# Performance work log

Measured on AMD Instinct MI355X. Metric: run time of the kernel, lower is better.

Reference implementation:

```python
import jax, jax.numpy as jnp
import numpy as np

EPS = 1e-5          # denominator epsilon from module
PROJ_EPS = 4e-3     # geoopt float32 projection epsilon
MIN_NORM = 1e-15


def _sabs(x):
    return jnp.abs(x) + MIN_NORM


def _sign(x):
    # geoopt sign: sign(0) == 1
    return jnp.sign(jnp.sign(x) + 0.5)


def _clamp_abs(x, eps):
    return _sign(x) * jnp.maximum(jnp.abs(x), eps)


def _lambda_x(x, k):
    # conformal factor 2 / (1 + k ||x||^2)
    return 2.0 / jnp.maximum(1.0 + k * jnp.sum(x * x, axis=-1, keepdims=True), MIN_NORM)


def _parallel_transport0back(x, v, k):
    # transport v at x back to the origin: v / (1 + k ||x||^2)
    return v / jnp.maximum(1.0 + k * jnp.sum(x * x, axis=-1, keepdims=True), MIN_NORM)


def _artan_k(x, k):
    sk = jnp.sqrt(_sabs(k))
    hyp = jnp.arctanh(jnp.minimum(sk * x, 1.0 - 1e-7)) / sk   # k < 0
    sph = jnp.arctan(sk * x) / sk                              # k > 0
    return jnp.where(k < 0, hyp, sph)


def _tan_k(x, k):
    sk = jnp.sqrt(_sabs(k))
    return jnp.where(k < 0, jnp.tanh(sk * x) / sk, jnp.tan(sk * x) / sk)


def _project(x, k):
    maxnorm = (1.0 - PROJ_EPS) / jnp.sqrt(_sabs(k))
    maxnorm = jnp.where(k < 0, maxnorm, 1e15)
    norm = jnp.maximum(jnp.linalg.norm(x, axis=-1, keepdims=True), MIN_NORM)
    return jnp.where(norm > maxnorm, x / norm * maxnorm, x)


def _mobius_scalar_mul(r, x, k):
    xn = jnp.maximum(jnp.linalg.norm(x, axis=-1, keepdims=True), MIN_NORM)
    return _tan_k(r * _artan_k(xn, k), k) * (x / xn)


def setup_inputs() -> dict:
    key = jax.random.key(0)
    kQ, kK, kV = jax.random.split(key, 3)
    B, H, N, D = 4, 16, 4096, 64
    Q = jax.random.normal(kQ, (B, H, N, D), dtype=jnp.float32)
    K = jax.random.normal(kK, (B, H, N, D), dtype=jnp.float32)
    # V holds points on the Poincare ball: scale so ||V|| < 1
    V = 0.05 * jax.random.normal(kV, (B, H, N, D), dtype=jnp.float32)
    mask = jnp.ones((N,), dtype=jnp.float32)
    c = jnp.array([-1.0], dtype=jnp.float32)  # hyperbolic curvature (geoopt k-convention)
    return {"Q": Q, "K": K, "V": V, "mask": mask, "c": c}


def reference(Q, K, V, mask, c):
    H = Q.shape[-3]
    curv = jnp.broadcast_to(c.reshape(-1), (H,)) if c.shape[0] == 1 else c
    curv = curv[:, None, None]  # [H,1,1] broadcasts over [B,H,N,D]

    x = V
    v1 = _parallel_transport0back(x, Q, curv)
    v2 = _parallel_transport0back(x, K, curv)
    gamma = _lambda_x(x, curv)                     # [B,H,N,1]
    denom = _clamp_abs(gamma - 1.0, 1e-10)
    m = mask[None, :, None]                        # [1,N,1]
    x = gamma / denom * x * m
    v1 = jax.nn.elu(v1) + 1.0
    v2 = denom * (jax.nn.elu(v2) + 1.0) * m

    v2_sum = jnp.sum(v2, axis=-2)                  # [B,H,D]
    D = jnp.einsum('...nd,...d->...n', v1, v2_sum)
    D_inv = 1.0 / jnp.where(D == 0, EPS, D)
    context = jnp.einsum('...nd,...ne->...de', v2, x)   # [B,H,D,D]
    X = jnp.einsum('...de,...nd,...n->...ne', context, v1, D_inv)

    X = _project(X, curv)
    X = _mobius_scalar_mul(0.5, X, curv)
    X = _project(X, curv)
    return X
```

## Files before the change

### kernel.cpp

```cpp
#include <hip/hip_runtime.h>
#include <math.h>

#define EPS_C      1e-05f
#define PROJ_EPS_C 0.004f
#define MIN_NORM_C 1e-15f

#define NTOK   4096
#define DH     64
#define CHUNK2 256
#define NCHUNK2 (NTOK / CHUNK2)
#define PADROW 68
#define SUB    16

#define FMA4(ACC, S, B)                      \
    ACC.x = fmaf((S), (B).x, ACC.x);         \
    ACC.y = fmaf((S), (B).y, ACC.y);         \
    ACC.z = fmaf((S), (B).z, ACC.z);         \
    ACC.w = fmaf((S), (B).w, ACC.w);

#define ADD4(ACC, B)                         \
    ACC.x += (B).x; ACC.y += (B).y;          \
    ACC.z += (B).z; ACC.w += (B).w;

#define LDS_FENCE() do {                                   \
    asm volatile("s_waitcnt lgkmcnt(0)" ::: "memory");     \
    __builtin_amdgcn_sched_barrier(0);                     \
} while (0)

__device__ __forceinline__ float elup(float z) {
    return z > 0.f ? z + 1.f : __expf(z);
}

__global__ __launch_bounds__(256, 3) void glin_phase1(
    const float* __restrict__ Kk, const float* __restrict__ Vv,
    const float* __restrict__ mask, const float* __restrict__ cc,
    int csize, int H, int chunk_toks, int BH,
    float* __restrict__ pt_out,
    float* __restrict__ part_v2, float* __restrict__ part_ctx)
{
    __shared__ __align__(16) float stg[4][2][SUB][PADROW];
    __shared__ __align__(16) float v2red[4][DH];

    const int bh    = blockIdx.x;
    const int chunk = blockIdx.y;
    const int h     = bh % H;
    const float k   = cc[(csize == 1) ? 0 : h];

    const float* Kp = Kk + (size_t)bh * NTOK * DH;
    const float* Vp = Vv + (size_t)bh * NTOK * DH;
    float* ptp      = pt_out + (size_t)bh * NTOK;

    const int tid  = threadIdx.x;
    const int w    = tid >> 6;
    const int lane = tid & 63;
    const int r    = lane >> 3;
    const int cg   = lane & 7;
    const int srow = lane >> 4;
    const int c4   = lane & 15;

    float (*v2w)[PADROW] = stg[w][0];
    float (*xsw)[PADROW] = stg[w][1];

    float4 acc[8][2];
#pragma unroll
    for (int i = 0; i < 8; ++i) {
        acc[i][0] = make_float4(0.f, 0.f, 0.f, 0.f);
        acc[i][1] = make_float4(0.f, 0.f, 0.f, 0.f);
    }
    float4 va0 = make_float4(0.f, 0.f, 0.f, 0.f);
    float4 va1 = make_float4(0.f, 0.f, 0.f, 0.f);

    const int wtok  = chunk_toks >> 2;
    const int wbase = chunk * chunk_toks + w * wtok;

    float4 pv0, pv1, pv2, pv3, pk0, pk1, pk2, pk3;
    float  pm0, pm1, pm2, pm3;

#define P1_LOAD(S) { \
    const float* vp_ = Vp + (size_t)(wbase + (S) + srow) * DH + c4 * 4; \
    const float* kp_ = Kp + (size_t)(wbase + (S) + srow) * DH + c4 * 4; \
    pv0 = *(const float4*)(vp_);            pk0 = *(const float4*)(kp_); \
    pv1 = *(const float4*)(vp_ + 4 * DH);   pk1 = *(const float4*)(kp_ + 4 * DH); \
    pv2 = *(const float4*)(vp_ + 8 * DH);   pk2 = *(const float4*)(kp_ + 8 * DH); \
    pv3 = *(const float4*)(vp_ + 12 * DH);  pk3 = *(const float4*)(kp_ + 12 * DH); \
    const float* mp_ = mask + wbase + (S) + srow; \
    pm0 = mp_[0]; pm1 = mp_[4]; pm2 = mp_[8]; pm3 = mp_[12]; \
}

#define P1_XF(PV, PK, PM, P, S) { \
    const int row_ = (P) * 4 + srow; \
    float ss = PV.x*PV.x + PV.y*PV.y + PV.z*PV.z + PV.w*PV.w; \
    ss += __shfl_xor(ss, 1); ss += __shfl_xor(ss, 2); \
    ss += __shfl_xor(ss, 4); ss += __shfl_xor(ss, 8); \
    const float dpt   = fmaxf(1.f + k * ss, MIN_NORM_C); \
    const float pt_   = 1.f / dpt; \
    const float gamma = 2.f * pt_; \
    const float gm1   = gamma - 1.f; \
    const float sg    = (gm1 < 0.f) ? -1.f : 1.f;    \
    const float denomG = sg * fmaxf(fabsf(gm1), 1e-10f); \
    const float xsc   = gamma / denomG * PM; \
    const float a2    = denomG * PM; \
    if (c4 == 0) ptp[wbase + (S) + row_] = pt_; \
    float4 xv; xv.x = PV.x*xsc; xv.y = PV.y*xsc; xv.z = PV.z*xsc; xv.w = PV.w*xsc; \
    float4 wv; wv.x = a2*elup(PK.x*pt_); wv.y = a2*elup(PK.y*pt_); \
               wv.z = a2*elup(PK.z*pt_); wv.w = a2*elup(PK.w*pt_); \
    *(float4*)&xsw[row_][c4 * 4] = xv; \
    *(float4*)&v2w[row_][c4 * 4] = wv; \
}

    P1_LOAD(0);
    for (int s = 0; s < wtok; s += SUB) {
        LDS_FENCE();
        P1_XF(pv0, pk0, pm0, 0, s);
        P1_XF(pv1, pk1, pm1, 1, s);
        P1_XF(pv2, pk2, pm2, 2, s);
        P1_XF(pv3, pk3, pm3, 3, s);
        if (s + SUB < wtok) P1_LOAD(s + SUB);
        LDS_FENCE();
#pragma unroll 4
        for (int t = 0; t < SUB; ++t) {
            const float4 a0 = *(const float4*)&v2w[t][r * 8];
            const float4 a1 = *(const float4*)&v2w[t][r * 8 + 4];
            const float4 b0 = *(const float4*)&xsw[t][cg * 8];
            const float4 b1 = *(const float4*)&xsw[t][cg * 8 + 4];
            ADD4(va0, a0);
            ADD4(va1, a1);
            FMA4(acc[0][0], a0.x, b0); FMA4(acc[0][1], a0.x, b1);
            FMA4(acc[1][0], a0.y, b0); FMA4(acc[1][1], a0.y, b1);
            FMA4(acc[2][0], a0.z, b0); FMA4(acc[2][1], a0.z, b1);
            FMA4(acc[3][0], a0.w, b0); FMA4(acc[3][1], a0.w, b1);
            FMA4(acc[4][0], a1.x, b0); FMA4(acc[4][1], a1.x, b1);
            FMA4(acc[5][0], a1.y, b0); FMA4(acc[5][1], a1.y, b1);
            FMA4(acc[6][0], a1.z, b0); FMA4(acc[6][1], a1.z, b1);
            FMA4(acc[7][0], a1.w, b0); FMA4(acc[7][1], a1.w, b1);
        }
    }

    if (cg == 0) {
        *(float4*)&v2red[w][r * 8]     = va0;
        *(float4*)&v2red[w][r * 8 + 4] = va1;
    }
    __syncthreads();

    float* red   = &stg[0][0][0][0];
    const int eo = cg * 8;
    if (w == 1) {
#pragma unroll
        for (int i = 0; i < 8; ++i) {
            *(float4*)&red[(r * 8 + i) * DH + eo]     = acc[i][0];
            *(float4*)&red[(r * 8 + i) * DH + eo + 4] = acc[i][1];
        }
    } else if (w == 3) {
#pragma unroll
        for (int i = 0; i < 8; ++i) {
            *(float4*)&red[4096 + (r * 8 + i) * DH + eo]     = acc[i][0];
            *(float4*)&red[4096 + (r * 8 + i) * DH + eo + 4] = acc[i][1];
        }
    }
    __syncthreads();
    if (w == 0) {
#pragma unroll
        for (int i = 0; i < 8; ++i) {
            float4 t0 = *(const float4*)&red[(r * 8 + i) * DH + eo];
            float4 t1 = *(const float4*)&red[(r * 8 + i) * DH + eo + 4];
            ADD4(acc[i][0], t0);
            ADD4(acc[i][1], t1);
        }
    } else if (w == 2) {
#pragma unroll
        for (int i = 0; i < 8; ++i) {
            float4 t0 = *(const float4*)&red[4096 + (r * 8 + i) * DH + eo];
            float4 t1 = *(const float4*)&red[4096 + (r * 8 + i) * DH + eo + 4];
            ADD4(acc[i][0], t0);
            ADD4(acc[i][1], t1);
        }
    } else if (w == 1) {
        float sv = v2red[0][lane] + v2red[1][lane] + v2red[2][lane] + v2red[3][lane];
        part_v2[((size_t)chunk * BH + bh) * DH + lane] = sv;
    }
    __syncthreads();
    if (w == 2) {
#pragma unroll
        for (int i = 0; i < 8; ++i) {
            *(float4*)&red[(r * 8 + i) * DH + eo]     = acc[i][0];
            *(float4*)&red[(r * 8 + i) * DH + eo + 4] = acc[i][1];
        }
    }
    __syncthreads();
    if (w == 0) {
        float* pc = part_ctx + ((size_t)chunk * BH + bh) * (DH * DH);
#pragma unroll
        for (int i = 0; i < 8; ++i) {
            float4 t0 = *(const float4*)&red[(r * 8 + i) * DH + eo];
            float4 t1 = *(const float4*)&red[(r * 8 + i) * DH + eo + 4];
            ADD4(acc[i][0], t0);
            ADD4(acc[i][1], t1);
            *(float4*)&pc[(r * 8 + i) * DH + eo]     = acc[i][0];
            *(float4*)&pc[(r * 8 + i) * DH + eo + 4] = acc[i][1];
        }
    }
}

__global__ __launch_bounds__(256) void glin_reduce(
    const float* __restrict__ part_ctx, const float* __restrict__ part_v2,
    int P, int BH,
    float* __restrict__ ctx_out, float* __restrict__ v2sum_out)
{
    const int bh   = blockIdx.x;
    const int q    = blockIdx.y;
    const int tid  = threadIdx.x;
    const int base = q * 256 + tid;

    float s0 = 0.f;
    for (int c = 0; c < P; ++c)
        s0 += part_ctx[((size_t)c * BH + bh) * (DH * DH) + base];
    ctx_out[(size_t)bh * DH * DH + base] = s0;

    if (q == 0 && tid < DH) {
        float s = 0.f;
        for (int c = 0; c < P; ++c)
            s += part_v2[((size_t)c * BH + bh) * DH + tid];
        v2sum_out[(size_t)bh * DH + tid] = s;
    }
}

__device__ __forceinline__ void epilogue_store(
    float4 x, float dv, float k, float sk, float maxnorm,
    float* __restrict__ outp, int gtok, int tx)
{
    x.x *= dv; x.y *= dv; x.z *= dv; x.w *= dv;
    float n2 = x.x * x.x + x.y * x.y + x.z * x.z + x.w * x.w;
    n2 += __shfl_xor(n2, 1);
    n2 += __shfl_xor(n2, 2);
    n2 += __shfl_xor(n2, 4);
    n2 += __shfl_xor(n2, 8);
    float n  = fmaxf(sqrtf(n2), MIN_NORM_C);
    float scale = 1.f;
    float n1 = n;
    if (n > maxnorm) { scale = maxnorm / n; n1 = maxnorm; }
    float xn = fmaxf(n1, MIN_NORM_C);
    float s2;
    if (k < 0.f) {
        float t = fminf(sk * xn, 1.f - 1e-7f);
        s2 = 1.f / (1.f + sqrtf(fmaxf(1.f - t * t, 0.f)));
    } else {
        float t = sk * xn;
        s2 = 1.f / (1.f + sqrtf(1.f + t * t));
    }
    scale *= s2;
    float nrm2 = fmaxf(n1 * s2, MIN_NORM_C);
    if (nrm2 > maxnorm) scale *= maxnorm / nrm2;
    float4 o;
    o.x = x.x * scale; o.y = x.y * scale;
    o.z = x.z * scale; o.w = x.w * scale;
    *(float4*)(outp + (size_t)gtok * DH + tx * 4) = o;
}

__global__ __launch_bounds__(256, 4) void glin_phase2(
    const float* __restrict__ Qq, const float* __restrict__ cc,
    int csize, int H,
    const float* __restrict__ pt_in, const float* __restrict__ v2sum_in,
    const float* __restrict__ ctx_in, float* __restrict__ out)
{
    __shared__ __align__(16) float ctxs[DH][PADROW];
    __shared__ __align__(16) float v1b[4][SUB][PADROW];
    __shared__ __align__(16) float v2sum[DH];
    __shared__ __align__(16) float dinvw[4][SUB];
    __shared__ __align__(16) float ptl[CHUNK2];

    const int bh    = blockIdx.x;
    const int chunk = blockIdx.y;
    const int h     = bh % H;
    const float k   = cc[(csize == 1) ? 0 : h];
    const float sk  = sqrtf(fabsf(k) + MIN_NORM_C);
    const float maxnorm = (k < 0.f) ? (1.f - PROJ_EPS_C) / sk : 1e15f;

    const int tid  = threadIdx.x;
    const int w    = tid >> 6;
    const int lane = tid & 63;
    const int ty   = lane >> 4;
    const int tx   = lane & 15;

    const float* Qp = Qq + (size_t)bh * NTOK * DH;
    float* outp     = out + (size_t)bh * NTOK * DH;

#pragma unroll
    for (int p = 0; p < 4; ++p) {
        int f = tid + p * 256;
        int d = f >> 4, e4 = f & 15;
        *(float4*)&ctxs[d][e4 * 4] =
            *(const float4*)(ctx_in + (size_t)bh * DH * DH + d * DH + e4 * 4);
    }
    if (tid < 16)
        *(float4*)&v2sum[tid * 4] =
            *(const float4*)(v2sum_in + (size_t)bh * DH + tid * 4);
    if (tid < CHUNK2 / 4)
        *(float4*)&ptl[tid * 4] =
            *(const float4*)(pt_in + (size_t)bh * NTOK + chunk * CHUNK2 + tid * 4);
    __syncthreads();

    const int wloc = w * (CHUNK2 / 4);
    const int wtb  = chunk * CHUNK2 + wloc;

    float4 qa0, qa1, qa2, qa3, qb0, qb1, qb2, qb3;

#define P2_LOADQ(R0, R1, R2, R3, S) { \
    const float* qp_ = Qp + (size_t)(wtb + (S) + ty) * DH + tx * 4; \
    R0 = *(const float4*)(qp_); \
    R1 = *(const float4*)(qp_ + 4 * DH); \
    R2 = *(const float4*)(qp_ + 8 * DH); \
    R3 = *(const float4*)(qp_ + 12 * DH); \
}

#define P2_BUILD(R, P, S) { \
    const int row_ = (P) * 4 + ty; \
    const float ptv = ptl[wloc + (S) + row_]; \
    float4 v1; \
    v1.x = elup(R.x * ptv); v1.y = elup(R.y * ptv); \
    v1.z = elup(R.z * ptv); v1.w = elup(R.w * ptv); \
    const float4 vs = *(const float4*)&v2sum[tx * 4]; \
    float dp = v1.x*vs.x + v1.y*vs.y + v1.z*vs.z + v1.w*vs.w; \
    dp += __shfl_xor(dp, 1); dp += __shfl_xor(dp, 2); \
    dp += __shfl_xor(dp, 4); dp += __shfl_xor(dp, 8); \
    if (tx == 0) dinvw[w][row_] = 1.f / ((dp == 0.f) ? EPS_C : dp); \
    *(float4*)&v1b[w][row_][tx * 4] = v1; \
}

#define P2_TILE(R0, R1, R2, R3, S) { \
     \
     \
    LDS_FENCE(); \
    P2_BUILD(R0, 0, S) P2_BUILD(R1, 1, S) P2_BUILD(R2, 2, S) P2_BUILD(R3, 3, S) \
    LDS_FENCE(); \
    float4 acc0 = make_float4(0.f, 0.f, 0.f, 0.f); \
    float4 acc1 = make_float4(0.f, 0.f, 0.f, 0.f); \
    float4 acc2 = make_float4(0.f, 0.f, 0.f, 0.f); \
    float4 acc3 = make_float4(0.f, 0.f, 0.f, 0.f); \
    _Pragma("unroll 8") \
    for (int db = 0; db < DH / 4; ++db) { \
        const float4 b0 = *(const float4*)&ctxs[db * 4 + 0][tx * 4]; \
        const float4 b1 = *(const float4*)&ctxs[db * 4 + 1][tx * 4]; \
        const float4 b2 = *(const float4*)&ctxs[db * 4 + 2][tx * 4]; \
        const float4 b3 = *(const float4*)&ctxs[db * 4 + 3][tx * 4]; \
        const float4 a0 = *(const float4*)&v1b[w][ty * 4 + 0][db * 4]; \
        FMA4(acc0, a0.x, b0); FMA4(acc0, a0.y, b1); FMA4(acc0, a0.z, b2); FMA4(acc0, a0.w, b3); \
        const float4 a1 = *(const float4*)&v1b[w][ty * 4 + 1][db * 4]; \
        FMA4(acc1, a1.x, b0); FMA4(acc1, a1.y, b1); FMA4(acc1, a1.z, b2); FMA4(acc1, a1.w, b3); \
        const float4 a2 = *(const float4*)&v1b[w][ty * 4 + 2][db * 4]; \
        FMA4(acc2, a2.x, b0); FMA4(acc2, a2.y, b1); FMA4(acc2, a2.z, b2); FMA4(acc2, a2.w, b3); \
        const float4 a3 = *(const float4*)&v1b[w][ty * 4 + 3][db * 4]; \
        FMA4(acc3, a3.x, b0); FMA4(acc3, a3.y, b1); FMA4(acc3, a3.z, b2); FMA4(acc3, a3.w, b3); \
    } \
    epilogue_store(acc0, dinvw[w][ty * 4 + 0], k, sk, maxnorm, outp, wtb + (S) + ty * 4 + 0, tx); \
    epilogue_store(acc1, dinvw[w][ty * 4 + 1], k, sk, maxnorm, outp, wtb + (S) + ty * 4 + 1, tx); \
    epilogue_store(acc2, dinvw[w][ty * 4 + 2], k, sk, maxnorm, outp, wtb + (S) + ty * 4 + 2, tx); \
    epilogue_store(acc3, dinvw[w][ty * 4 + 3], k, sk, maxnorm, outp, wtb + (S) + ty * 4 + 3, tx); \
}

    P2_LOADQ(qa0, qa1, qa2, qa3, 0);
    P2_LOADQ(qb0, qb1, qb2, qb3, SUB);
    P2_TILE (qa0, qa1, qa2, qa3, 0);
    P2_LOADQ(qa0, qa1, qa2, qa3, 2 * SUB);
    P2_TILE (qb0, qb1, qb2, qb3, SUB);
    P2_LOADQ(qb0, qb1, qb2, qb3, 3 * SUB);
    P2_TILE (qa0, qa1, qa2, qa3, 2 * SUB);
    P2_TILE (qb0, qb1, qb2, qb3, 3 * SUB);
}

extern "C" void kernel_launch(void* const* d_in, const int* in_sizes, int n_in,
                              void* d_out, int out_size, void* d_ws, size_t ws_size,
                              hipStream_t stream)
{
    const float* Q    = (const float*)d_in[0];
    const float* K    = (const float*)d_in[1];
    const float* V    = (const float*)d_in[2];
    const float* mask = (const float*)d_in[3];
    const float* c    = (const float*)d_in[4];
    const int csize   = in_sizes[4];
    const int BH      = in_sizes[0] / (NTOK * DH);
    const int H       = 16;
    float* out        = (float*)d_out;

    int P = 16;
    while (P > 1) {
        size_t need = ((size_t)BH * NTOK
                     + (size_t)BH * DH
                     + (size_t)BH * DH * DH
                     + (size_t)P * BH * DH
                     + (size_t)P * BH * DH * DH)
                     * sizeof(float);
        if (need <= ws_size) break;
        P >>= 1;
    }
    const int chunk_toks = NTOK / P;

    float* pt       = (float*)d_ws;
    float* v2sum    = pt + (size_t)BH * NTOK;
    float* ctx      = v2sum + (size_t)BH * DH;
    float* part_v2  = ctx + (size_t)BH * DH * DH;
    float* part_ctx = part_v2 + (size_t)P * BH * DH;

    dim3 g1(BH, P);
    glin_phase1<<<g1, 256, 0, stream>>>(K, V, mask, c, csize, H, chunk_toks, BH,
                                        pt, part_v2, part_ctx);
    dim3 gr(BH, 16);
    glin_reduce<<<gr, 16 * sizeof(float) * 0 + 256, 0, stream>>>(part_ctx, part_v2, P, BH, ctx, v2sum);
    dim3 g2(BH, NCHUNK2);
    glin_phase2<<<g2, 256, 0, stream>>>(Q, c, csize, H, pt, v2sum, ctx, out);
}
```

Measured before the change: 268.2 us.

## Stage K/V tiles into LDS via global_load_lds with double buffering in phase1

Phase 1 now streams K and V tiles of 8 tokens straight from global memory into per-wave LDS double buffers using the direct global-to-LDS load builtin. The next tile is prefetched while the current one is transformed in place and accumulated. This replaces the register-prefetch scheme and is meant to cut register pressure, which allows the launch bound to rise from 3 to 4 blocks per CU. The risks are more frequent fences and vmcnt waits from the smaller tiles, and possible LDS bank conflicts, because the rows are no longer padded.

```diff
diff --git a/kernel.cpp b/kernel.cpp
--- a/kernel.cpp
+++ b/kernel.cpp
@@ -11,6 +11,7 @@
 #define NCHUNK2 (NTOK / CHUNK2)
 #define PADROW 68
 #define SUB    16
+#define TS     8
 
 #define FMA4(ACC, S, B)                      \
     ACC.x = fmaf((S), (B).x, ACC.x);         \
@@ -31,14 +32,24 @@
     return z > 0.f ? z + 1.f : __expf(z);
 }
 
-__global__ __launch_bounds__(256, 3) void glin_phase1(
+typedef __attribute__((address_space(1))) void glob_void;
+typedef __attribute__((address_space(3))) void lds_void;
+
+__device__ __forceinline__ void gl_lds16(const float* g, float* l) {
+    __builtin_amdgcn_global_load_lds(
+        (glob_void*)(uintptr_t)g,
+        (lds_void*)(uint32_t)(uintptr_t)l,
+        16, 0, 0);
+}
+
+__global__ __launch_bounds__(256, 4) void glin_phase1(
     const float* __restrict__ Kk, const float* __restrict__ Vv,
     const float* __restrict__ mask, const float* __restrict__ cc,
     int csize, int H, int chunk_toks, int BH,
     float* __restrict__ pt_out,
     float* __restrict__ part_v2, float* __restrict__ part_ctx)
 {
-    __shared__ __align__(16) float stg[4][2][SUB][PADROW];
+    __shared__ __align__(16) float kvbuf[4][2][2][TS][DH];
     __shared__ __align__(16) float v2red[4][DH];
 
     const int bh    = blockIdx.x;
@@ -58,8 +69,7 @@
     const int srow = lane >> 4;
     const int c4   = lane & 15;
 
-    float (*v2w)[PADROW] = stg[w][0];
-    float (*xsw)[PADROW] = stg[w][1];
+    float* wbuf = &kvbuf[w][0][0][0][0];
 
     float4 acc[8][2];
 #pragma unroll
@@ -72,24 +82,33 @@
 
     const int wtok  = chunk_toks >> 2;
     const int wbase = chunk * chunk_toks + w * wtok;
-
-    float4 pv0, pv1, pv2, pv3, pk0, pk1, pk2, pk3;
-    float  pm0, pm1, pm2, pm3;
-
-#define P1_LOAD(S) { \
-    const float* vp_ = Vp + (size_t)(wbase + (S) + srow) * DH + c4 * 4; \
-    const float* kp_ = Kp + (size_t)(wbase + (S) + srow) * DH + c4 * 4; \
-    pv0 = *(const float4*)(vp_);            pk0 = *(const float4*)(kp_); \
-    pv1 = *(const float4*)(vp_ + 4 * DH);   pk1 = *(const float4*)(kp_ + 4 * DH); \
-    pv2 = *(const float4*)(vp_ + 8 * DH);   pk2 = *(const float4*)(kp_ + 8 * DH); \
-    pv3 = *(const float4*)(vp_ + 12 * DH);  pk3 = *(const float4*)(kp_ + 12 * DH); \
-    const float* mp_ = mask + wbase + (S) + srow; \
-    pm0 = mp_[0]; pm1 = mp_[4]; pm2 = mp_[8]; pm3 = mp_[12]; \
-}
-
-#define P1_XF(PV, PK, PM, P, S) { \
+    const int nt    = wtok / TS;
+
+    float pm0, pm1;
+
+#define P1_STAGE(T, CUR) { \
+    const float* gk_ = Kp + (size_t)(wbase + (T) * TS) * DH + lane * 4; \
+    const float* gv_ = Vp + (size_t)(wbase + (T) * TS) * DH + lane * 4; \
+    float* lk_ = wbuf + (CUR) * 1024; \
+    float* lv_ = wbuf + (CUR) * 1024 + 512; \
+    gl_lds16(gk_,       lk_); \
+    gl_lds16(gk_ + 256, lk_ + 256); \
+    gl_lds16(gv_,       lv_); \
+    gl_lds16(gv_ + 256, lv_ + 256); \
+}
+
+#define P1_PM(T) { \
+    pm0 = mask[wbase + (T) * TS + srow]; \
+    pm1 = mask[wbase + (T) * TS + 4 + srow]; \
+}
+
+#define P1_XF(P, T, PM) { \
     const int row_ = (P) * 4 + srow; \
-    float ss = PV.x*PV.x + PV.y*PV.y + PV.z*PV.z + PV.w*PV.w; \
+    float* lk_ = wbuf + cur * 1024 + (P) * 256 + lane * 4; \
+    float* lv_ = wbuf + cur * 1024 + 512 + (P) * 256 + lane * 4; \
+    float4 v4 = *(const float4*)lv_; \
+    float4 k4 = *(const float4*)lk_; \
+    float ss = v4.x*v4.x + v4.y*v4.y + v4.z*v4.z + v4.w*v4.w; \
     ss += __shfl_xor(ss, 1); ss += __shfl_xor(ss, 2); \
     ss += __shfl_xor(ss, 4); ss += __shfl_xor(ss, 8); \
     const float dpt   = fmaxf(1.f + k * ss, MIN_NORM_C); \
@@ -98,31 +117,42 @@
     const float gm1   = gamma - 1.f; \
     const float sg    = (gm1 < 0.f) ? -1.f : 1.f;    \
     const float denomG = sg * fmaxf(fabsf(gm1), 1e-10f); \
-    const float xsc   = gamma / denomG * PM; \
-    const float a2    = denomG * PM; \
-    if (c4 == 0) ptp[wbase + (S) + row_] = pt_; \
-    float4 xv; xv.x = PV.x*xsc; xv.y = PV.y*xsc; xv.z = PV.z*xsc; xv.w = PV.w*xsc; \
-    float4 wv; wv.x = a2*elup(PK.x*pt_); wv.y = a2*elup(PK.y*pt_); \
-               wv.z = a2*elup(PK.z*pt_); wv.w = a2*elup(PK.w*pt_); \
-    *(float4*)&xsw[row_][c4 * 4] = xv; \
-    *(float4*)&v2w[row_][c4 * 4] = wv; \
-}
-
-    P1_LOAD(0);
-    for (int s = 0; s < wtok; s += SUB) {
+    const float xsc   = gamma / denomG * (PM); \
+    const float a2    = denomG * (PM); \
+    if (c4 == 0) ptp[wbase + (T) * TS + row_] = pt_; \
+    float4 xv; xv.x = v4.x*xsc; xv.y = v4.y*xsc; xv.z = v4.z*xsc; xv.w = v4.w*xsc; \
+    float4 wv; wv.x = a2*elup(k4.x*pt_); wv.y = a2*elup(k4.y*pt_); \
+               wv.z = a2*elup(k4.z*pt_); wv.w = a2*elup(k4.w*pt_); \
+    *(float4*)lv_ = xv; \
+    *(float4*)lk_ = wv; \
+}
+
+    P1_STAGE(0, 0);
+    P1_PM(0);
+    int cur = 0;
+
+    for (int t = 0; t < nt; ++t) {
         LDS_FENCE();
-        P1_XF(pv0, pk0, pm0, 0, s);
-        P1_XF(pv1, pk1, pm1, 1, s);
-        P1_XF(pv2, pk2, pm2, 2, s);
-        P1_XF(pv3, pk3, pm3, 3, s);
-        if (s + SUB < wtok) P1_LOAD(s + SUB);
+        const int nxt = cur ^ 1;
+        if (t + 1 < nt) {
+            P1_STAGE(t + 1, nxt);
+            asm volatile("s_waitcnt vmcnt(4)" ::: "memory");
+        } else {
+            asm volatile("s_waitcnt vmcnt(0)" ::: "memory");
+        }
+        __builtin_amdgcn_sched_barrier(0);
+        P1_XF(0, t, pm0);
+        P1_XF(1, t, pm1);
+        if (t + 1 < nt) P1_PM(t + 1);
         LDS_FENCE();
-#pragma unroll 4
-        for (int t = 0; t < SUB; ++t) {
-            const float4 a0 = *(const float4*)&v2w[t][r * 8];
-            const float4 a1 = *(const float4*)&v2w[t][r * 8 + 4];
-            const float4 b0 = *(const float4*)&xsw[t][cg * 8];
-            const float4 b1 = *(const float4*)&xsw[t][cg * 8 + 4];
+        const float* bk = wbuf + cur * 1024;
+        const float* bv = wbuf + cur * 1024 + 512;
+#pragma unroll
+        for (int tt = 0; tt < TS; ++tt) {
+            const float4 a0 = *(const float4*)(bk + tt * DH + r * 8);
+            const float4 a1 = *(const float4*)(bk + tt * DH + r * 8 + 4);
+            const float4 b0 = *(const float4*)(bv + tt * DH + cg * 8);
+            const float4 b1 = *(const float4*)(bv + tt * DH + cg * 8 + 4);
             ADD4(va0, a0);
             ADD4(va1, a1);
             FMA4(acc[0][0], a0.x, b0); FMA4(acc[0][1], a0.x, b1);
@@ -134,6 +164,7 @@
             FMA4(acc[6][0], a1.z, b0); FMA4(acc[6][1], a1.z, b1);
             FMA4(acc[7][0], a1.w, b0); FMA4(acc[7][1], a1.w, b1);
         }
+        cur ^= 1;
     }
 
     if (cg == 0) {
@@ -142,7 +173,7 @@
     }
     __syncthreads();
 
-    float* red   = &stg[0][0][0][0];
+    float* red   = &kvbuf[0][0][0][0][0];
     const int eo = cg * 8;
     if (w == 1) {
 #pragma unroll
@@ -327,8 +358,6 @@
 }
 
 #define P2_TILE(R0, R1, R2, R3, S) { \
-     \
-     \
     LDS_FENCE(); \
     P2_BUILD(R0, 0, S) P2_BUILD(R1, 1, S) P2_BUILD(R2, 2, S) P2_BUILD(R3, 3, S) \
     LDS_FENCE(); \
@@ -404,7 +433,7 @@
     glin_phase1<<<g1, 256, 0, stream>>>(K, V, mask, c, csize, H, chunk_toks, BH,
                                         pt, part_v2, part_ctx);
     dim3 gr(BH, 16);
-    glin_reduce<<<gr, 16 * sizeof(float) * 0 + 256, 0, stream>>>(part_ctx, part_v2, P, BH, ctx, v2sum);
+    glin_reduce<<<gr, 256, 0, stream>>>(part_ctx, part_v2, P, BH, ctx, v2sum);
     dim3 g2(BH, NCHUNK2);
     glin_phase2<<<g2, 256, 0, stream>>>(Q, c, csize, H, pt, v2sum, ctx, out);
 }
```

After: 317.5 us. +18.4%, slower.
